# Kernel tuning notes

Hardware: AMD Instinct MI355X
Metric: run time of the kernel (lower is better)

Reference implementation:

```python
import jax, jax.numpy as jnp
import numpy as np

N_NODES = 200000
N_EDGES = 3200000
N_GRAPHS = 4096
IN_CH = 78
H1, H2, OUT_DIM = 64, 128, 128


def setup_inputs() -> dict:
    key = jax.random.key(0)
    ks = jax.random.split(key, 10)
    x = jax.random.normal(ks[0], (N_NODES, IN_CH), dtype=jnp.float32)
    edge_index = jax.random.randint(ks[1], (2, N_EDGES), 0, N_NODES, dtype=jnp.int64)
    batch = jnp.sort(jax.random.randint(ks[2], (N_NODES,), 0, N_GRAPHS, dtype=jnp.int64))
    # GCNConv weights (PyG: lin has no bias by default; conv bias added after aggregation)
    def glorot(k, fan_in, fan_out):
        lim = jnp.sqrt(6.0 / (fan_in + fan_out)).astype(jnp.float32)
        return jax.random.uniform(k, (fan_in, fan_out), jnp.float32, -lim, lim)
    W1 = glorot(ks[3], IN_CH, H1)
    b1 = jnp.zeros((H1,), jnp.float32)
    W2 = glorot(ks[4], H1, H2)
    b2 = jnp.zeros((H2,), jnp.float32)
    fc_w = glorot(ks[5], H2, OUT_DIM)
    fc_b = jnp.zeros((OUT_DIM,), jnp.float32)
    return {"x": x, "edge_index": edge_index, "batch": batch,
            "W1": W1, "b1": b1, "W2": W2, "b2": b2, "fc_w": fc_w, "fc_b": fc_b}


def _gcn_forward(x, edge_index, batch, W1, b1, W2, b2, fc_w, fc_b):
    N = x.shape[0]
    # GCNConv default: add self loops, symmetric deg^-1/2 normalization
    self_loops = jnp.arange(N, dtype=edge_index.dtype)
    src = jnp.concatenate([edge_index[0], self_loops])  # [E+N]
    dst = jnp.concatenate([edge_index[1], self_loops])  # [E+N]
    deg = jax.ops.segment_sum(jnp.ones_like(dst, dtype=jnp.float32), dst,
                              num_segments=N)  # in-degree incl self loop
    dinv = jnp.where(deg > 0, jax.lax.rsqrt(jnp.maximum(deg, 1.0)), 0.0)
    norm = dinv[src] * dinv[dst]  # [E+N]

    def gcn_layer(h, W, b):
        hw = h @ W                              # transform first (small dims)
        msg = hw[src] * norm[:, None]           # gather + scale  [E+N, F]
        agg = jax.ops.segment_sum(msg, dst, num_segments=N)  # scatter-add
        return agg + b

    h = jax.nn.relu(gcn_layer(x, W1, b1))
    h = jax.nn.relu(gcn_layer(h, W2, b2))
    # global_mean_pool over per-graph segments
    counts = jax.ops.segment_sum(jnp.ones((N,), jnp.float32), batch,
                                 num_segments=N_GRAPHS)
    pooled = jax.ops.segment_sum(h, batch, num_segments=N_GRAPHS)
    pooled = pooled / jnp.maximum(counts, 1.0)[:, None]  # [G, H2]
    return pooled @ fc_w + fc_b                           # [G, OUT_DIM]


def reference(x, edge_index, batch, W1, b1, W2, b2, fc_w, fc_b):
    return _gcn_forward(x, edge_index, batch, W1, b1, W2, b2, fc_w, fc_b)
```

## Files before the change

kernel.cpp:

```cpp
#include <hip/hip_runtime.h>
#include <hip/hip_bf16.h>

#define NN 200000
#define NE 3200000
#define NG 4096
#define INC 78
#define C1 64
#define C2 128
#define ODIM 128
#define KP1 96

#define BSZ 256
#define NBKT 782
#define NBLK 196
#define EPB 16327
#define SCN (NBKT*NBLK)
#define MAXREC 12288

using bf16 = __hip_bfloat16;
typedef __attribute__((ext_vector_type(8))) short bf16x8;
typedef __attribute__((ext_vector_type(4))) float f32x4;

static inline size_t alignup(size_t x) { return (x + 255) & ~size_t(255); }

__device__ __forceinline__ float bflo(unsigned u) { return __uint_as_float(u << 16); }
__device__ __forceinline__ float bfhi(unsigned u) { return __uint_as_float(u & 0xffff0000u); }
__device__ __forceinline__ unsigned short f2bf(float f) {
    __hip_bfloat16 h = __float2bfloat16(f);
    return *reinterpret_cast<unsigned short*>(&h);
}

__global__ void hist1_kernel(const int* __restrict__ dst, int* __restrict__ histM) {
    __shared__ int lh[NBKT];
    for (int j = threadIdx.x; j < NBKT; j += 256) lh[j] = 0;
    __syncthreads();
    int e0 = blockIdx.x * EPB;
    int e1 = e0 + EPB; if (e1 > NE) e1 = NE;
    for (int e = e0 + threadIdx.x; e < e1; e += 256)
        atomicAdd(&lh[((unsigned)dst[e]) >> 8], 1);
    __syncthreads();
    for (int j = threadIdx.x; j < NBKT; j += 256)
        histM[j * NBLK + blockIdx.x] = lh[j];
}

__global__ void scan1_kernel(int* __restrict__ data, int* __restrict__ bsum, int n) {
    __shared__ int tmp[256];
    int tid = threadIdx.x, gid = blockIdx.x * 256 + tid;
    int v = (gid < n) ? data[gid] : 0;
    tmp[tid] = v;
    __syncthreads();
    for (int off = 1; off < 256; off <<= 1) {
        int t = (tid >= off) ? tmp[tid - off] : 0;
        __syncthreads();
        tmp[tid] += t;
        __syncthreads();
    }
    if (gid < n) data[gid] = tmp[tid] - v;
    if (tid == 255) bsum[blockIdx.x] = tmp[255];
}

__global__ void scan2_kernel(int* __restrict__ bsum, int nb) {
    __shared__ int tmp[1024];
    int tid = threadIdx.x;
    int v = (tid < nb) ? bsum[tid] : 0;
    tmp[tid] = v;
    __syncthreads();
    for (int off = 1; off < 1024; off <<= 1) {
        int t = (tid >= off) ? tmp[tid - off] : 0;
        __syncthreads();
        tmp[tid] += t;
        __syncthreads();
    }
    if (tid < nb) bsum[tid] = tmp[tid] - v;
}

__global__ void scatter2_kernel(const int* __restrict__ src, const int* __restrict__ dst,
                                const int* __restrict__ histM, const int* __restrict__ bsum,
                                unsigned* __restrict__ ecsr) {
    __shared__ int lc[NBKT];
    for (int j = threadIdx.x; j < NBKT; j += 256) {
        int idx = j * NBLK + blockIdx.x;
        lc[j] = histM[idx] + bsum[idx >> 8];
    }
    __syncthreads();
    int e0 = blockIdx.x * EPB;
    int e1 = e0 + EPB; if (e1 > NE) e1 = NE;
    for (int e = e0 + threadIdx.x; e < e1; e += 256) {
        int d = dst[e];
        int s = src[e];
        int pos = atomicAdd(&lc[((unsigned)d) >> 8], 1);
        ecsr[pos] = ((unsigned)s << 8) | (unsigned)(d & 255);
    }
}

__global__ __launch_bounds__(256) void degcsr_kernel(
    const int* __restrict__ histM, const int* __restrict__ bsum,
    int* __restrict__ rs, float* __restrict__ dinv, unsigned* __restrict__ ecsr) {
    __shared__ int cnt[BSZ];
    __shared__ int pfx[BSZ];
    __shared__ unsigned recs[MAXREC];
    int b = blockIdx.x;
    int i0 = b * NBLK;
    int s0 = histM[i0] + bsum[i0 >> 8];
    int s1 = NE;
    if (b + 1 < NBKT) {
        int i1 = (b + 1) * NBLK;
        s1 = histM[i1] + bsum[i1 >> 8];
    }
    int nrec = s1 - s0;
    if (nrec > MAXREC) nrec = MAXREC;
    cnt[threadIdx.x] = 0;
    for (int i = threadIdx.x; i < nrec; i += 256) recs[i] = ecsr[s0 + i];
    __syncthreads();
    for (int i = threadIdx.x; i < nrec; i += 256)
        atomicAdd(&cnt[recs[i] & 255], 1);
    __syncthreads();
    int v = cnt[threadIdx.x];
    pfx[threadIdx.x] = v;
    __syncthreads();
    for (int off = 1; off < 256; off <<= 1) {
        int t = (threadIdx.x >= off) ? pfx[threadIdx.x - off] : 0;
        __syncthreads();
        pfx[threadIdx.x] += t;
        __syncthreads();
    }
    int myrs = s0 + pfx[threadIdx.x] - v;
    int node = b * BSZ + threadIdx.x;
    if (node < NN) {
        rs[node] = myrs;
        dinv[node] = rsqrtf((float)v + 1.0f);
    }
    if (node == NN) rs[NN] = NE;
    __syncthreads();
    cnt[threadIdx.x] = 0;
    pfx[threadIdx.x] = myrs;
    __syncthreads();
    for (int i = threadIdx.x; i < nrec; i += 256) {
        unsigned rec = recs[i];
        int nl = rec & 255;
        int pos = atomicAdd(&cnt[nl], 1);
        ecsr[pfx[nl] + pos] = rec >> 8;
    }
}

__global__ void convw2_kernel(const float* __restrict__ W1, const float* __restrict__ W2,
                              unsigned short* __restrict__ Wt1, unsigned short* __restrict__ Wt2) {
    int idx = blockIdx.x * 256 + threadIdx.x;
    if (idx < C1 * KP1) {
        int c = idx / KP1, k = idx % KP1;
        Wt1[idx] = f2bf((k < INC) ? W1[k * C1 + c] : 0.f);
    } else {
        int j = idx - C1 * KP1;
        if (j < C2 * C1) {
            int c = j / C1, k = j % C1;
            Wt2[j] = f2bf(W2[k * C2 + c]);
        }
    }
}

__global__ __launch_bounds__(256) void gemm1_mfma(const float* __restrict__ x,
                                                  const unsigned short* __restrict__ Wt1,
                                                  const float* __restrict__ dinv,
                                                  unsigned short* __restrict__ hw1s) {
    __shared__ float xs[64 * INC];
    const float4* gsrc = (const float4*)(x + (size_t)blockIdx.x * 64 * INC);
    float4* ldst = (float4*)xs;
    #pragma unroll
    for (int t = 0; t < 5; ++t) {
        int i = t * 256 + threadIdx.x;
        if (i < (64 * INC) / 4) ldst[i] = gsrc[i];
    }
    __syncthreads();
    int wave = threadIdx.x >> 6, lane = threadIdx.x & 63;
    int r = lane & 15, kg = lane >> 4;
    int lrow = wave * 16 + r;
    int row0 = blockIdx.x * 64 + wave * 16;
    const float* arow = xs + lrow * INC;
    bf16x8 a[3];
    #pragma unroll
    for (int t = 0; t < 3; ++t) {
        union { bf16x8 v; unsigned short u[8]; } tmp;
        #pragma unroll
        for (int j = 0; j < 8; ++j) {
            int k = t * 32 + kg * 8 + j;
            tmp.u[j] = (k < INC) ? f2bf(arow[k]) : (unsigned short)0;
        }
        a[t] = tmp.v;
    }
    float dsc[4];
    #pragma unroll
    for (int i = 0; i < 4; ++i) dsc[i] = dinv[row0 + kg * 4 + i];
    #pragma unroll
    for (int nt = 0; nt < 4; ++nt) {
        const unsigned short* wrow = Wt1 + (size_t)(nt * 16 + r) * KP1 + kg * 8;
        bf16x8 b0 = *(const bf16x8*)(wrow);
        bf16x8 b1 = *(const bf16x8*)(wrow + 32);
        bf16x8 b2 = *(const bf16x8*)(wrow + 64);
        f32x4 acc = {0.f, 0.f, 0.f, 0.f};
        acc = __builtin_amdgcn_mfma_f32_16x16x32_bf16(a[0], b0, acc, 0, 0, 0);
        acc = __builtin_amdgcn_mfma_f32_16x16x32_bf16(a[1], b1, acc, 0, 0, 0);
        acc = __builtin_amdgcn_mfma_f32_16x16x32_bf16(a[2], b2, acc, 0, 0, 0);
        unsigned short* cb = hw1s + (size_t)(row0 + kg * 4) * C1 + nt * 16 + r;
        #pragma unroll
        for (int i = 0; i < 4; ++i) cb[(size_t)i * C1] = f2bf(acc[i] * dsc[i]);
    }
}

__device__ __forceinline__ void gather_node(
    const unsigned* __restrict__ csr, int start, int len,
    const unsigned short* __restrict__ vin, int c0,
    float& a0, float& a1, float& a2, float& a3,
    float& a4, float& a5, float& a6, float& a7) {
    int e = 0;
    for (; e + 4 <= len; e += 4) {
        unsigned s0 = csr[start + e + 0];
        unsigned s1 = csr[start + e + 1];
        unsigned s2 = csr[start + e + 2];
        unsigned s3 = csr[start + e + 3];
        uint4 r0 = *(const uint4*)(vin + (size_t)s0 * 64 + c0);
        uint4 r1 = *(const uint4*)(vin + (size_t)s1 * 64 + c0);
        uint4 r2 = *(const uint4*)(vin + (size_t)s2 * 64 + c0);
        uint4 r3 = *(const uint4*)(vin + (size_t)s3 * 64 + c0);
        a0 += (bflo(r0.x) + bflo(r1.x)) + (bflo(r2.x) + bflo(r3.x));
        a1 += (bfhi(r0.x) + bfhi(r1.x)) + (bfhi(r2.x) + bfhi(r3.x));
        a2 += (bflo(r0.y) + bflo(r1.y)) + (bflo(r2.y) + bflo(r3.y));
        a3 += (bfhi(r0.y) + bfhi(r1.y)) + (bfhi(r2.y) + bfhi(r3.y));
        a4 += (bflo(r0.z) + bflo(r1.z)) + (bflo(r2.z) + bflo(r3.z));
        a5 += (bfhi(r0.z) + bfhi(r1.z)) + (bfhi(r2.z) + bfhi(r3.z));
        a6 += (bflo(r0.w) + bflo(r1.w)) + (bflo(r2.w) + bflo(r3.w));
        a7 += (bfhi(r0.w) + bfhi(r1.w)) + (bfhi(r2.w) + bfhi(r3.w));
    }
    for (; e < len; ++e) {
        unsigned s = csr[start + e];
        uint4 ra = *(const uint4*)(vin + (size_t)s * 64 + c0);
        a0 += bflo(ra.x); a1 += bfhi(ra.x);
        a2 += bflo(ra.y); a3 += bfhi(ra.y);
        a4 += bflo(ra.z); a5 += bfhi(ra.z);
        a6 += bflo(ra.w); a7 += bfhi(ra.w);
    }
}

__global__ __launch_bounds__(256) void agg1_kernel(
    const unsigned* __restrict__ csr, const int* __restrict__ rs,
    const float* __restrict__ dinv, const unsigned short* __restrict__ vin,
    const float* __restrict__ bias, unsigned short* __restrict__ vout) {
    int node = blockIdx.x * 32 + (threadIdx.x >> 3);
    int l = threadIdx.x & 7;
    int c0 = l * 8;
    int start = rs[node], len = rs[node + 1] - start;
    float a0 = 0.f, a1 = 0.f, a2 = 0.f, a3 = 0.f, a4 = 0.f, a5 = 0.f, a6 = 0.f, a7 = 0.f;
    gather_node(csr, start, len, vin, c0, a0, a1, a2, a3, a4, a5, a6, a7);
    uint4 sv = *(const uint4*)(vin + (size_t)node * 64 + c0);
    a0 += bflo(sv.x); a1 += bfhi(sv.x);
    a2 += bflo(sv.y); a3 += bfhi(sv.y);
    a4 += bflo(sv.z); a5 += bfhi(sv.z);
    a6 += bflo(sv.w); a7 += bfhi(sv.w);
    float d = dinv[node];
    a0 = fmaxf(a0 * d + bias[c0 + 0], 0.f) * d;
    a1 = fmaxf(a1 * d + bias[c0 + 1], 0.f) * d;
    a2 = fmaxf(a2 * d + bias[c0 + 2], 0.f) * d;
    a3 = fmaxf(a3 * d + bias[c0 + 3], 0.f) * d;
    a4 = fmaxf(a4 * d + bias[c0 + 4], 0.f) * d;
    a5 = fmaxf(a5 * d + bias[c0 + 5], 0.f) * d;
    a6 = fmaxf(a6 * d + bias[c0 + 6], 0.f) * d;
    a7 = fmaxf(a7 * d + bias[c0 + 7], 0.f) * d;
    uint4 o;
    o.x = (unsigned)f2bf(a0) | ((unsigned)f2bf(a1) << 16);
    o.y = (unsigned)f2bf(a2) | ((unsigned)f2bf(a3) << 16);
    o.z = (unsigned)f2bf(a4) | ((unsigned)f2bf(a5) << 16);
    o.w = (unsigned)f2bf(a6) | ((unsigned)f2bf(a7) << 16);
    *(uint4*)(vout + (size_t)node * 64 + c0) = o;
}

__global__ __launch_bounds__(256) void agg2g_mfma(
    const unsigned* __restrict__ csr, const int* __restrict__ rs,
    const float* __restrict__ dinv, const unsigned short* __restrict__ h1s,
    const unsigned short* __restrict__ Wt2, const float* __restrict__ b2,
    unsigned short* __restrict__ h2) {
    __shared__ unsigned short A[64 * 72];
    int grp = threadIdx.x >> 3;
    int l = threadIdx.x & 7;
    int c0 = l * 8;
    #pragma unroll
    for (int half = 0; half < 2; ++half) {
        int nl = grp + half * 32;
        int node = blockIdx.x * 64 + nl;
        int start = rs[node], len = rs[node + 1] - start;
        float a0 = 0.f, a1 = 0.f, a2 = 0.f, a3 = 0.f, a4 = 0.f, a5 = 0.f, a6 = 0.f, a7 = 0.f;
        gather_node(csr, start, len, h1s, c0, a0, a1, a2, a3, a4, a5, a6, a7);
        uint4 sv = *(const uint4*)(h1s + (size_t)node * 64 + c0);
        a0 += bflo(sv.x); a1 += bfhi(sv.x);
        a2 += bflo(sv.y); a3 += bfhi(sv.y);
        a4 += bflo(sv.z); a5 += bfhi(sv.z);
        a6 += bflo(sv.w); a7 += bfhi(sv.w);
        float d = dinv[node];
        uint4 o;
        o.x = (unsigned)f2bf(a0 * d) | ((unsigned)f2bf(a1 * d) << 16);
        o.y = (unsigned)f2bf(a2 * d) | ((unsigned)f2bf(a3 * d) << 16);
        o.z = (unsigned)f2bf(a4 * d) | ((unsigned)f2bf(a5 * d) << 16);
        o.w = (unsigned)f2bf(a6 * d) | ((unsigned)f2bf(a7 * d) << 16);
        *(uint4*)(A + nl * 72 + c0) = o;
    }
    __syncthreads();
    int wave = threadIdx.x >> 6, lane = threadIdx.x & 63;
    int r = lane & 15, kg = lane >> 4;
    int lrow = wave * 16 + r;
    int row0 = blockIdx.x * 64 + wave * 16;
    bf16x8 a0 = *(const bf16x8*)(A + lrow * 72 + kg * 8);
    bf16x8 a1 = *(const bf16x8*)(A + lrow * 72 + 32 + kg * 8);
    #pragma unroll
    for (int nt = 0; nt < 8; ++nt) {
        const unsigned short* wrow = Wt2 + (size_t)(nt * 16 + r) * C1 + kg * 8;
        bf16x8 b0 = *(const bf16x8*)(wrow);
        bf16x8 b1 = *(const bf16x8*)(wrow + 32);
        f32x4 acc = {0.f, 0.f, 0.f, 0.f};
        acc = __builtin_amdgcn_mfma_f32_16x16x32_bf16(a0, b0, acc, 0, 0, 0);
        acc = __builtin_amdgcn_mfma_f32_16x16x32_bf16(a1, b1, acc, 0, 0, 0);
        int col = nt * 16 + r;
        float bb = b2[col];
        unsigned short* cb = h2 + (size_t)(row0 + kg * 4) * C2 + col;
        #pragma unroll
        for (int i = 0; i < 4; ++i) cb[(size_t)i * C2] = f2bf(fmaxf(acc[i] + bb, 0.f));
    }
}

__device__ __forceinline__ int lbound(const int* __restrict__ a, int n, int key) {
    int lo = 0, hi = n;
    while (lo < hi) {
        int mid = (lo + hi) >> 1;
        if (a[mid] < key) lo = mid + 1; else hi = mid;
    }
    return lo;
}

__global__ __launch_bounds__(256) void pool_fc_kernel(const unsigned short* __restrict__ h2,
                                                      const int* __restrict__ batch,
                                                      const float* __restrict__ fcw,
                                                      const float* __restrict__ fcb,
                                                      float* __restrict__ out) {
    __shared__ float ps[512];
    __shared__ float pr[128];
    int g = blockIdx.x;
    int lo = lbound(batch, NN, g);
    int hi = lbound(batch, NN, g + 1);
    int cnt = hi - lo;
    int rg = threadIdx.x >> 6;
    int p = threadIdx.x & 63;
    float s0 = 0.f, s1 = 0.f;
    for (int r = lo + rg; r < hi; r += 4) {
        unsigned v = *(const unsigned*)(h2 + (size_t)r * C2 + p * 2);
        s0 += bflo(v);
        s1 += bfhi(v);
    }
    ps[threadIdx.x * 2 + 0] = s0;
    ps[threadIdx.x * 2 + 1] = s1;
    __syncthreads();
    if (threadIdx.x < 64) {
        float inv = 1.0f / (float)((cnt > 0) ? cnt : 1);
        int t = threadIdx.x;
        float r0 = 0.f, r1 = 0.f;
        #pragma unroll
        for (int k = 0; k < 4; ++k) {
            r0 += ps[(k * 64 + t) * 2 + 0];
            r1 += ps[(k * 64 + t) * 2 + 1];
        }
        pr[2 * t + 0] = r0 * inv;
        pr[2 * t + 1] = r1 * inv;
    }
    __syncthreads();
    if (threadIdx.x < 128) {
        int o = threadIdx.x;
        float acc = fcb[o];
        #pragma unroll 8
        for (int k = 0; k < C2; ++k) acc += pr[k] * fcw[k * ODIM + o];
        out[(size_t)g * ODIM + o] = acc;
    }
}

extern "C" void kernel_launch(void* const* d_in, const int* in_sizes, int n_in,
                              void* d_out, int out_size, void* d_ws, size_t ws_size,
                              hipStream_t stream) {
    const float* x   = (const float*)d_in[0];
    const int*   ei  = (const int*)d_in[1];
    const int*   bat = (const int*)d_in[2];
    const float* W1  = (const float*)d_in[3];
    const float* b1  = (const float*)d_in[4];
    const float* W2  = (const float*)d_in[5];
    const float* b2  = (const float*)d_in[6];
    const float* fcw = (const float*)d_in[7];
    const float* fcb = (const float*)d_in[8];
    float* out = (float*)d_out;

    const int* src = ei;
    const int* dst = ei + NE;

    char* ws = (char*)d_ws;
    int* histM   = (int*)ws;            ws += alignup((size_t)SCN * 4);
    int* bsum    = (int*)ws;            ws += alignup(1024 * 4);
    int* rs      = (int*)ws;            ws += alignup((size_t)(NN + 1) * 4);
    float* dinv  = (float*)ws;          ws += alignup((size_t)NN * 4);
    unsigned short* Wt1 = (unsigned short*)ws;  ws += alignup((size_t)C1 * KP1 * 2);
    unsigned short* Wt2 = (unsigned short*)ws;  ws += alignup((size_t)C2 * C1 * 2);
    unsigned short* hw1s = (unsigned short*)ws; ws += alignup((size_t)NN * C1 * 2);
    unsigned* ecsr = (unsigned*)ws;     ws += alignup((size_t)NE * 4);
    unsigned short* h1s = (unsigned short*)ws;  ws += alignup((size_t)NN * C1 * 2);
    unsigned short* h2 = (unsigned short*)ws;   ws += alignup((size_t)NN * C2 * 2);

    hist1_kernel<<<NBLK, 256, 0, stream>>>(dst, histM);
    const int SCB = (SCN + 255) / 256;
    scan1_kernel<<<SCB, 256, 0, stream>>>(histM, bsum, SCN);
    scan2_kernel<<<1, 1024, 0, stream>>>(bsum, SCB);
    scatter2_kernel<<<NBLK, 256, 0, stream>>>(src, dst, histM, bsum, ecsr);

    degcsr_kernel<<<NBKT, 256, 0, stream>>>(histM, bsum, rs, dinv, ecsr);

    convw2_kernel<<<(C1 * KP1 + C2 * C1 + 255) / 256, 256, 0, stream>>>(W1, W2, Wt1, Wt2);

    gemm1_mfma<<<NN / 64, 256, 0, stream>>>(x, Wt1, dinv, hw1s);
    agg1_kernel<<<NN / 32, 256, 0, stream>>>(ecsr, rs, dinv, hw1s, b1, h1s);

    agg2g_mfma<<<NN / 64, 256, 0, stream>>>(ecsr, rs, dinv, h1s, Wt2, b2, h2);

    pool_fc_kernel<<<NG, 256, 0, stream>>>(h2, bat, fcw, fcb, out);
}
```

Measured before the change: 299.7 us.

## Split 64-channel features into two 32-channel halves mapped to XCD groups

Node features are stored as two separate 32-column bf16 arrays. The aggregation kernels pick a half from the XCD index of the block (blockIdx & 7), so each group of four XCDs gathers from a working set half the size, which should fit better in its L2. The second layer's aggregation is split out of the fused agg+GEMM kernel into a separate half-aggregation pass and a standalone GEMM2 kernel. This adds an extra kernel launch and a round trip of the aggregated features through global memory, and it relies on the hardware assigning blocks to XCDs round-robin.

```diff
diff --git a/kernel.cpp b/kernel.cpp
--- a/kernel.cpp
+++ b/kernel.cpp
@@ -16,6 +16,7 @@
 #define EPB 16327
 #define SCN (NBKT*NBLK)
 #define MAXREC 12288
+#define HGRID 6256
 
 using bf16 = __hip_bfloat16;
 typedef __attribute__((ext_vector_type(8))) short bf16x8;
@@ -161,7 +162,8 @@
 __global__ __launch_bounds__(256) void gemm1_mfma(const float* __restrict__ x,
                                                   const unsigned short* __restrict__ Wt1,
                                                   const float* __restrict__ dinv,
-                                                  unsigned short* __restrict__ hw1s) {
+                                                  unsigned short* __restrict__ hwA,
+                                                  unsigned short* __restrict__ hwB) {
     __shared__ float xs[64 * INC];
     const float4* gsrc = (const float4*)(x + (size_t)blockIdx.x * 64 * INC);
     float4* ldst = (float4*)xs;
@@ -200,13 +202,15 @@
         acc = __builtin_amdgcn_mfma_f32_16x16x32_bf16(a[0], b0, acc, 0, 0, 0);
         acc = __builtin_amdgcn_mfma_f32_16x16x32_bf16(a[1], b1, acc, 0, 0, 0);
         acc = __builtin_amdgcn_mfma_f32_16x16x32_bf16(a[2], b2, acc, 0, 0, 0);
-        unsigned short* cb = hw1s + (size_t)(row0 + kg * 4) * C1 + nt * 16 + r;
+        int col = nt * 16 + r;
+        unsigned short* tb = (col < 32) ? hwA : hwB;
+        unsigned short* cb = tb + (size_t)(row0 + kg * 4) * 32 + (col & 31);
         #pragma unroll
-        for (int i = 0; i < 4; ++i) cb[(size_t)i * C1] = f2bf(acc[i] * dsc[i]);
-    }
-}
-
-__device__ __forceinline__ void gather_node(
+        for (int i = 0; i < 4; ++i) cb[(size_t)i * 32] = f2bf(acc[i] * dsc[i]);
+    }
+}
+
+__device__ __forceinline__ void gather32(
     const unsigned* __restrict__ csr, int start, int len,
     const unsigned short* __restrict__ vin, int c0,
     float& a0, float& a1, float& a2, float& a3,
@@ -217,10 +221,10 @@
         unsigned s1 = csr[start + e + 1];
         unsigned s2 = csr[start + e + 2];
         unsigned s3 = csr[start + e + 3];
-        uint4 r0 = *(const uint4*)(vin + (size_t)s0 * 64 + c0);
-        uint4 r1 = *(const uint4*)(vin + (size_t)s1 * 64 + c0);
-        uint4 r2 = *(const uint4*)(vin + (size_t)s2 * 64 + c0);
-        uint4 r3 = *(const uint4*)(vin + (size_t)s3 * 64 + c0);
+        uint4 r0 = *(const uint4*)(vin + (size_t)s0 * 32 + c0);
+        uint4 r1 = *(const uint4*)(vin + (size_t)s1 * 32 + c0);
+        uint4 r2 = *(const uint4*)(vin + (size_t)s2 * 32 + c0);
+        uint4 r3 = *(const uint4*)(vin + (size_t)s3 * 32 + c0);
         a0 += (bflo(r0.x) + bflo(r1.x)) + (bflo(r2.x) + bflo(r3.x));
         a1 += (bfhi(r0.x) + bfhi(r1.x)) + (bfhi(r2.x) + bfhi(r3.x));
         a2 += (bflo(r0.y) + bflo(r1.y)) + (bflo(r2.y) + bflo(r3.y));
@@ -232,7 +236,7 @@
     }
     for (; e < len; ++e) {
         unsigned s = csr[start + e];
-        uint4 ra = *(const uint4*)(vin + (size_t)s * 64 + c0);
+        uint4 ra = *(const uint4*)(vin + (size_t)s * 32 + c0);
         a0 += bflo(ra.x); a1 += bfhi(ra.x);
         a2 += bflo(ra.y); a3 += bfhi(ra.y);
         a4 += bflo(ra.z); a5 += bfhi(ra.z);
@@ -240,74 +244,61 @@
     }
 }
 
-__global__ __launch_bounds__(256) void agg1_kernel(
+template <int EP>
+__global__ __launch_bounds__(256) void agg_half_kernel(
     const unsigned* __restrict__ csr, const int* __restrict__ rs,
-    const float* __restrict__ dinv, const unsigned short* __restrict__ vin,
-    const float* __restrict__ bias, unsigned short* __restrict__ vout) {
-    int node = blockIdx.x * 32 + (threadIdx.x >> 3);
-    int l = threadIdx.x & 7;
-    int c0 = l * 8;
+    const float* __restrict__ dinv,
+    const unsigned short* __restrict__ vinA, const unsigned short* __restrict__ vinB,
+    const float* __restrict__ bias,
+    unsigned short* __restrict__ voutA, unsigned short* __restrict__ voutB) {
+    int xcd = blockIdx.x & 7;
+    int half = xcd >> 2;
+    int ord = (blockIdx.x >> 3) * 4 + (xcd & 3);
+    int node = ord * 64 + (threadIdx.x >> 2);
+    if (node >= NN) return;
+    int c0 = (threadIdx.x & 3) * 8;
+    const unsigned short* vin = half ? vinB : vinA;
+    unsigned short* vout = half ? voutB : voutA;
     int start = rs[node], len = rs[node + 1] - start;
     float a0 = 0.f, a1 = 0.f, a2 = 0.f, a3 = 0.f, a4 = 0.f, a5 = 0.f, a6 = 0.f, a7 = 0.f;
-    gather_node(csr, start, len, vin, c0, a0, a1, a2, a3, a4, a5, a6, a7);
-    uint4 sv = *(const uint4*)(vin + (size_t)node * 64 + c0);
+    gather32(csr, start, len, vin, c0, a0, a1, a2, a3, a4, a5, a6, a7);
+    uint4 sv = *(const uint4*)(vin + (size_t)node * 32 + c0);
     a0 += bflo(sv.x); a1 += bfhi(sv.x);
     a2 += bflo(sv.y); a3 += bfhi(sv.y);
     a4 += bflo(sv.z); a5 += bfhi(sv.z);
     a6 += bflo(sv.w); a7 += bfhi(sv.w);
     float d = dinv[node];
-    a0 = fmaxf(a0 * d + bias[c0 + 0], 0.f) * d;
-    a1 = fmaxf(a1 * d + bias[c0 + 1], 0.f) * d;
-    a2 = fmaxf(a2 * d + bias[c0 + 2], 0.f) * d;
-    a3 = fmaxf(a3 * d + bias[c0 + 3], 0.f) * d;
-    a4 = fmaxf(a4 * d + bias[c0 + 4], 0.f) * d;
-    a5 = fmaxf(a5 * d + bias[c0 + 5], 0.f) * d;
-    a6 = fmaxf(a6 * d + bias[c0 + 6], 0.f) * d;
-    a7 = fmaxf(a7 * d + bias[c0 + 7], 0.f) * d;
+    if (EP == 1) {
+        const float* bb = bias + half * 32 + c0;
+        a0 = fmaxf(a0 * d + bb[0], 0.f) * d;
+        a1 = fmaxf(a1 * d + bb[1], 0.f) * d;
+        a2 = fmaxf(a2 * d + bb[2], 0.f) * d;
+        a3 = fmaxf(a3 * d + bb[3], 0.f) * d;
+        a4 = fmaxf(a4 * d + bb[4], 0.f) * d;
+        a5 = fmaxf(a5 * d + bb[5], 0.f) * d;
+        a6 = fmaxf(a6 * d + bb[6], 0.f) * d;
+        a7 = fmaxf(a7 * d + bb[7], 0.f) * d;
+    } else {
+        a0 *= d; a1 *= d; a2 *= d; a3 *= d; a4 *= d; a5 *= d; a6 *= d; a7 *= d;
+    }
     uint4 o;
     o.x = (unsigned)f2bf(a0) | ((unsigned)f2bf(a1) << 16);
     o.y = (unsigned)f2bf(a2) | ((unsigned)f2bf(a3) << 16);
     o.z = (unsigned)f2bf(a4) | ((unsigned)f2bf(a5) << 16);
     o.w = (unsigned)f2bf(a6) | ((unsigned)f2bf(a7) << 16);
-    *(uint4*)(vout + (size_t)node * 64 + c0) = o;
-}
-
-__global__ __launch_bounds__(256) void agg2g_mfma(
-    const unsigned* __restrict__ csr, const int* __restrict__ rs,
-    const float* __restrict__ dinv, const unsigned short* __restrict__ h1s,
-    const unsigned short* __restrict__ Wt2, const float* __restrict__ b2,
-    unsigned short* __restrict__ h2) {
-    __shared__ unsigned short A[64 * 72];
-    int grp = threadIdx.x >> 3;
-    int l = threadIdx.x & 7;
-    int c0 = l * 8;
-    #pragma unroll
-    for (int half = 0; half < 2; ++half) {
-        int nl = grp + half * 32;
-        int node = blockIdx.x * 64 + nl;
-        int start = rs[node], len = rs[node + 1] - start;
-        float a0 = 0.f, a1 = 0.f, a2 = 0.f, a3 = 0.f, a4 = 0.f, a5 = 0.f, a6 = 0.f, a7 = 0.f;
-        gather_node(csr, start, len, h1s, c0, a0, a1, a2, a3, a4, a5, a6, a7);
-        uint4 sv = *(const uint4*)(h1s + (size_t)node * 64 + c0);
-        a0 += bflo(sv.x); a1 += bfhi(sv.x);
-        a2 += bflo(sv.y); a3 += bfhi(sv.y);
-        a4 += bflo(sv.z); a5 += bfhi(sv.z);
-        a6 += bflo(sv.w); a7 += bfhi(sv.w);
-        float d = dinv[node];
-        uint4 o;
-        o.x = (unsigned)f2bf(a0 * d) | ((unsigned)f2bf(a1 * d) << 16);
-        o.y = (unsigned)f2bf(a2 * d) | ((unsigned)f2bf(a3 * d) << 16);
-        o.z = (unsigned)f2bf(a4 * d) | ((unsigned)f2bf(a5 * d) << 16);
-        o.w = (unsigned)f2bf(a6 * d) | ((unsigned)f2bf(a7 * d) << 16);
-        *(uint4*)(A + nl * 72 + c0) = o;
-    }
-    __syncthreads();
+    *(uint4*)(vout + (size_t)node * 32 + c0) = o;
+}
+
+__global__ __launch_bounds__(256) void gemm2_mfma(const unsigned short* __restrict__ aggA,
+                                                  const unsigned short* __restrict__ aggB,
+                                                  const unsigned short* __restrict__ Wt2,
+                                                  const float* __restrict__ b2,
+                                                  unsigned short* __restrict__ h2) {
     int wave = threadIdx.x >> 6, lane = threadIdx.x & 63;
     int r = lane & 15, kg = lane >> 4;
-    int lrow = wave * 16 + r;
     int row0 = blockIdx.x * 64 + wave * 16;
-    bf16x8 a0 = *(const bf16x8*)(A + lrow * 72 + kg * 8);
-    bf16x8 a1 = *(const bf16x8*)(A + lrow * 72 + 32 + kg * 8);
+    bf16x8 a0 = *(const bf16x8*)(aggA + (size_t)(row0 + r) * 32 + kg * 8);
+    bf16x8 a1 = *(const bf16x8*)(aggB + (size_t)(row0 + r) * 32 + kg * 8);
     #pragma unroll
     for (int nt = 0; nt < 8; ++nt) {
         const unsigned short* wrow = Wt2 + (size_t)(nt * 16 + r) * C1 + kg * 8;
@@ -401,9 +392,13 @@
     float* dinv  = (float*)ws;          ws += alignup((size_t)NN * 4);
     unsigned short* Wt1 = (unsigned short*)ws;  ws += alignup((size_t)C1 * KP1 * 2);
     unsigned short* Wt2 = (unsigned short*)ws;  ws += alignup((size_t)C2 * C1 * 2);
-    unsigned short* hw1s = (unsigned short*)ws; ws += alignup((size_t)NN * C1 * 2);
+    unsigned short* hw1sA = (unsigned short*)ws; ws += alignup((size_t)NN * 32 * 2);
+    unsigned short* hw1sB = (unsigned short*)ws; ws += alignup((size_t)NN * 32 * 2);
+    unsigned short* aggHA = hw1sA;
+    unsigned short* aggHB = hw1sB;
     unsigned* ecsr = (unsigned*)ws;     ws += alignup((size_t)NE * 4);
-    unsigned short* h1s = (unsigned short*)ws;  ws += alignup((size_t)NN * C1 * 2);
+    unsigned short* h1sA = (unsigned short*)ws; ws += alignup((size_t)NN * 32 * 2);
+    unsigned short* h1sB = (unsigned short*)ws; ws += alignup((size_t)NN * 32 * 2);
     unsigned short* h2 = (unsigned short*)ws;   ws += alignup((size_t)NN * C2 * 2);
 
     hist1_kernel<<<NBLK, 256, 0, stream>>>(dst, histM);
@@ -416,10 +411,11 @@
 
     convw2_kernel<<<(C1 * KP1 + C2 * C1 + 255) / 256, 256, 0, stream>>>(W1, W2, Wt1, Wt2);
 
-    gemm1_mfma<<<NN / 64, 256, 0, stream>>>(x, Wt1, dinv, hw1s);
-    agg1_kernel<<<NN / 32, 256, 0, stream>>>(ecsr, rs, dinv, hw1s, b1, h1s);
-
-    agg2g_mfma<<<NN / 64, 256, 0, stream>>>(ecsr, rs, dinv, h1s, Wt2, b2, h2);
+    gemm1_mfma<<<NN / 64, 256, 0, stream>>>(x, Wt1, dinv, hw1sA, hw1sB);
+    agg_half_kernel<1><<<HGRID, 256, 0, stream>>>(ecsr, rs, dinv, hw1sA, hw1sB, b1, h1sA, h1sB);
+
+    agg_half_kernel<2><<<HGRID, 256, 0, stream>>>(ecsr, rs, dinv, h1sA, h1sB, b1, aggHA, aggHB);
+    gemm2_mfma<<<NN / 64, 256, 0, stream>>>(aggHA, aggHB, Wt2, b2, h2);
 
     pool_fc_kernel<<<NG, 256, 0, stream>>>(h2, bat, fcw, fcb, out);
 }
```

After: 378.9 us. 1.26x slower.

## Replace histogram-scan CSR build with single-pass bucket binsort; split agg2 from GEMM2

Applied to the files above, without the earlier changes.

The multi-kernel CSR build (block histogram, two-level scan, scatter) is replaced by one binsort kernel. It stages edges in LDS, reserves space per bucket with global atomics, and writes into fixed-capacity per-bucket buffers, followed by a small bucket scan. The fused layer-2 gather+MFMA kernel is split into a reusable aggregation kernel and a standalone GEMM2 kernel that reads the aggregated bf16 features from global memory. The build saves launches and one pass over the edges, but gives up deterministic edge order and truncates any bucket above CAP=8192. The split adds a global write and read of the aggregated features.

```diff
diff --git a/kernel.cpp b/kernel.cpp
--- a/kernel.cpp
+++ b/kernel.cpp
@@ -12,10 +12,9 @@
 
 #define BSZ 256
 #define NBKT 782
-#define NBLK 196
-#define EPB 16327
-#define SCN (NBKT*NBLK)
-#define MAXREC 12288
+#define NBLK 392
+#define EPB 8164
+#define CAP 8192
 
 using bf16 = __hip_bfloat16;
 typedef __attribute__((ext_vector_type(8))) short bf16x8;
@@ -30,39 +29,43 @@
     return *reinterpret_cast<unsigned short*>(&h);
 }
 
-__global__ void hist1_kernel(const int* __restrict__ dst, int* __restrict__ histM) {
+__global__ __launch_bounds__(256) void binsort_kernel(const int* __restrict__ src,
+                                                      const int* __restrict__ dst,
+                                                      int* __restrict__ gcursor,
+                                                      unsigned* __restrict__ ebuf) {
+    __shared__ unsigned recs[EPB + 28];
+    __shared__ unsigned short bkts[EPB + 28];
     __shared__ int lh[NBKT];
     for (int j = threadIdx.x; j < NBKT; j += 256) lh[j] = 0;
     __syncthreads();
     int e0 = blockIdx.x * EPB;
     int e1 = e0 + EPB; if (e1 > NE) e1 = NE;
-    for (int e = e0 + threadIdx.x; e < e1; e += 256)
-        atomicAdd(&lh[((unsigned)dst[e]) >> 8], 1);
-    __syncthreads();
-    for (int j = threadIdx.x; j < NBKT; j += 256)
-        histM[j * NBLK + blockIdx.x] = lh[j];
-}
-
-__global__ void scan1_kernel(int* __restrict__ data, int* __restrict__ bsum, int n) {
-    __shared__ int tmp[256];
-    int tid = threadIdx.x, gid = blockIdx.x * 256 + tid;
-    int v = (gid < n) ? data[gid] : 0;
-    tmp[tid] = v;
-    __syncthreads();
-    for (int off = 1; off < 256; off <<= 1) {
-        int t = (tid >= off) ? tmp[tid - off] : 0;
-        __syncthreads();
-        tmp[tid] += t;
-        __syncthreads();
-    }
-    if (gid < n) data[gid] = tmp[tid] - v;
-    if (tid == 255) bsum[blockIdx.x] = tmp[255];
-}
-
-__global__ void scan2_kernel(int* __restrict__ bsum, int nb) {
+    int n = e1 - e0;
+    for (int i = threadIdx.x; i < n; i += 256) {
+        int d = dst[e0 + i];
+        int s = src[e0 + i];
+        recs[i] = ((unsigned)s << 8) | (unsigned)(d & 255);
+        int b = ((unsigned)d) >> 8;
+        bkts[i] = (unsigned short)b;
+        atomicAdd(&lh[b], 1);
+    }
+    __syncthreads();
+    for (int j = threadIdx.x; j < NBKT; j += 256) {
+        int c = lh[j];
+        lh[j] = (c > 0) ? atomicAdd(&gcursor[j], c) : 0;
+    }
+    __syncthreads();
+    for (int i = threadIdx.x; i < n; i += 256) {
+        int b = bkts[i];
+        int off = atomicAdd(&lh[b], 1);
+        if (off < CAP) ebuf[(size_t)b * CAP + off] = recs[i];
+    }
+}
+
+__global__ void bucketscan_kernel(const int* __restrict__ gcursor, int* __restrict__ bstart) {
     __shared__ int tmp[1024];
     int tid = threadIdx.x;
-    int v = (tid < nb) ? bsum[tid] : 0;
+    int v = (tid < NBKT) ? gcursor[tid] : 0;
     tmp[tid] = v;
     __syncthreads();
     for (int off = 1; off < 1024; off <<= 1) {
@@ -71,46 +74,22 @@
         tmp[tid] += t;
         __syncthreads();
     }
-    if (tid < nb) bsum[tid] = tmp[tid] - v;
-}
-
-__global__ void scatter2_kernel(const int* __restrict__ src, const int* __restrict__ dst,
-                                const int* __restrict__ histM, const int* __restrict__ bsum,
-                                unsigned* __restrict__ ecsr) {
-    __shared__ int lc[NBKT];
-    for (int j = threadIdx.x; j < NBKT; j += 256) {
-        int idx = j * NBLK + blockIdx.x;
-        lc[j] = histM[idx] + bsum[idx >> 8];
-    }
-    __syncthreads();
-    int e0 = blockIdx.x * EPB;
-    int e1 = e0 + EPB; if (e1 > NE) e1 = NE;
-    for (int e = e0 + threadIdx.x; e < e1; e += 256) {
-        int d = dst[e];
-        int s = src[e];
-        int pos = atomicAdd(&lc[((unsigned)d) >> 8], 1);
-        ecsr[pos] = ((unsigned)s << 8) | (unsigned)(d & 255);
-    }
+    if (tid < NBKT) bstart[tid] = tmp[tid] - v;
+    if (tid == NBKT) bstart[NBKT] = NE;
 }
 
 __global__ __launch_bounds__(256) void degcsr_kernel(
-    const int* __restrict__ histM, const int* __restrict__ bsum,
-    int* __restrict__ rs, float* __restrict__ dinv, unsigned* __restrict__ ecsr) {
+    const unsigned* __restrict__ ebuf, const int* __restrict__ gcursor,
+    const int* __restrict__ bstart, int* __restrict__ rs, float* __restrict__ dinv,
+    unsigned* __restrict__ csr) {
     __shared__ int cnt[BSZ];
     __shared__ int pfx[BSZ];
-    __shared__ unsigned recs[MAXREC];
+    __shared__ unsigned recs[CAP];
     int b = blockIdx.x;
-    int i0 = b * NBLK;
-    int s0 = histM[i0] + bsum[i0 >> 8];
-    int s1 = NE;
-    if (b + 1 < NBKT) {
-        int i1 = (b + 1) * NBLK;
-        s1 = histM[i1] + bsum[i1 >> 8];
-    }
-    int nrec = s1 - s0;
-    if (nrec > MAXREC) nrec = MAXREC;
+    int nrec = gcursor[b]; if (nrec > CAP) nrec = CAP;
+    int s0 = bstart[b];
     cnt[threadIdx.x] = 0;
-    for (int i = threadIdx.x; i < nrec; i += 256) recs[i] = ecsr[s0 + i];
+    for (int i = threadIdx.x; i < nrec; i += 256) recs[i] = ebuf[(size_t)b * CAP + i];
     __syncthreads();
     for (int i = threadIdx.x; i < nrec; i += 256)
         atomicAdd(&cnt[recs[i] & 255], 1);
@@ -139,7 +118,7 @@
         unsigned rec = recs[i];
         int nl = rec & 255;
         int pos = atomicAdd(&cnt[nl], 1);
-        ecsr[pfx[nl] + pos] = rec >> 8;
+        csr[pfx[nl] + pos] = rec >> 8;
     }
 }
 
@@ -240,7 +219,8 @@
     }
 }
 
-__global__ __launch_bounds__(256) void agg1_kernel(
+template <int EP>
+__global__ __launch_bounds__(256) void agg_csr_kernel(
     const unsigned* __restrict__ csr, const int* __restrict__ rs,
     const float* __restrict__ dinv, const unsigned short* __restrict__ vin,
     const float* __restrict__ bias, unsigned short* __restrict__ vout) {
@@ -256,14 +236,18 @@
     a4 += bflo(sv.z); a5 += bfhi(sv.z);
     a6 += bflo(sv.w); a7 += bfhi(sv.w);
     float d = dinv[node];
-    a0 = fmaxf(a0 * d + bias[c0 + 0], 0.f) * d;
-    a1 = fmaxf(a1 * d + bias[c0 + 1], 0.f) * d;
-    a2 = fmaxf(a2 * d + bias[c0 + 2], 0.f) * d;
-    a3 = fmaxf(a3 * d + bias[c0 + 3], 0.f) * d;
-    a4 = fmaxf(a4 * d + bias[c0 + 4], 0.f) * d;
-    a5 = fmaxf(a5 * d + bias[c0 + 5], 0.f) * d;
-    a6 = fmaxf(a6 * d + bias[c0 + 6], 0.f) * d;
-    a7 = fmaxf(a7 * d + bias[c0 + 7], 0.f) * d;
+    if (EP == 1) {
+        a0 = fmaxf(a0 * d + bias[c0 + 0], 0.f) * d;
+        a1 = fmaxf(a1 * d + bias[c0 + 1], 0.f) * d;
+        a2 = fmaxf(a2 * d + bias[c0 + 2], 0.f) * d;
+        a3 = fmaxf(a3 * d + bias[c0 + 3], 0.f) * d;
+        a4 = fmaxf(a4 * d + bias[c0 + 4], 0.f) * d;
+        a5 = fmaxf(a5 * d + bias[c0 + 5], 0.f) * d;
+        a6 = fmaxf(a6 * d + bias[c0 + 6], 0.f) * d;
+        a7 = fmaxf(a7 * d + bias[c0 + 7], 0.f) * d;
+    } else {
+        a0 *= d; a1 *= d; a2 *= d; a3 *= d; a4 *= d; a5 *= d; a6 *= d; a7 *= d;
+    }
     uint4 o;
     o.x = (unsigned)f2bf(a0) | ((unsigned)f2bf(a1) << 16);
     o.y = (unsigned)f2bf(a2) | ((unsigned)f2bf(a3) << 16);
@@ -272,42 +256,16 @@
     *(uint4*)(vout + (size_t)node * 64 + c0) = o;
 }
 
-__global__ __launch_bounds__(256) void agg2g_mfma(
-    const unsigned* __restrict__ csr, const int* __restrict__ rs,
-    const float* __restrict__ dinv, const unsigned short* __restrict__ h1s,
-    const unsigned short* __restrict__ Wt2, const float* __restrict__ b2,
-    unsigned short* __restrict__ h2) {
-    __shared__ unsigned short A[64 * 72];
-    int grp = threadIdx.x >> 3;
-    int l = threadIdx.x & 7;
-    int c0 = l * 8;
-    #pragma unroll
-    for (int half = 0; half < 2; ++half) {
-        int nl = grp + half * 32;
-        int node = blockIdx.x * 64 + nl;
-        int start = rs[node], len = rs[node + 1] - start;
-        float a0 = 0.f, a1 = 0.f, a2 = 0.f, a3 = 0.f, a4 = 0.f, a5 = 0.f, a6 = 0.f, a7 = 0.f;
-        gather_node(csr, start, len, h1s, c0, a0, a1, a2, a3, a4, a5, a6, a7);
-        uint4 sv = *(const uint4*)(h1s + (size_t)node * 64 + c0);
-        a0 += bflo(sv.x); a1 += bfhi(sv.x);
-        a2 += bflo(sv.y); a3 += bfhi(sv.y);
-        a4 += bflo(sv.z); a5 += bfhi(sv.z);
-        a6 += bflo(sv.w); a7 += bfhi(sv.w);
-        float d = dinv[node];
-        uint4 o;
-        o.x = (unsigned)f2bf(a0 * d) | ((unsigned)f2bf(a1 * d) << 16);
-        o.y = (unsigned)f2bf(a2 * d) | ((unsigned)f2bf(a3 * d) << 16);
-        o.z = (unsigned)f2bf(a4 * d) | ((unsigned)f2bf(a5 * d) << 16);
-        o.w = (unsigned)f2bf(a6 * d) | ((unsigned)f2bf(a7 * d) << 16);
-        *(uint4*)(A + nl * 72 + c0) = o;
-    }
-    __syncthreads();
+__global__ __launch_bounds__(256) void gemm2_mfma(const unsigned short* __restrict__ aggH,
+                                                  const unsigned short* __restrict__ Wt2,
+                                                  const float* __restrict__ b2,
+                                                  unsigned short* __restrict__ h2) {
     int wave = threadIdx.x >> 6, lane = threadIdx.x & 63;
     int r = lane & 15, kg = lane >> 4;
-    int lrow = wave * 16 + r;
     int row0 = blockIdx.x * 64 + wave * 16;
-    bf16x8 a0 = *(const bf16x8*)(A + lrow * 72 + kg * 8);
-    bf16x8 a1 = *(const bf16x8*)(A + lrow * 72 + 32 + kg * 8);
+    const unsigned short* arow = aggH + (size_t)(row0 + r) * 64 + kg * 8;
+    bf16x8 a0 = *(const bf16x8*)(arow);
+    bf16x8 a1 = *(const bf16x8*)(arow + 32);
     #pragma unroll
     for (int nt = 0; nt < 8; ++nt) {
         const unsigned short* wrow = Wt2 + (size_t)(nt * 16 + r) * C1 + kg * 8;
@@ -395,31 +353,32 @@
     const int* dst = ei + NE;
 
     char* ws = (char*)d_ws;
-    int* histM   = (int*)ws;            ws += alignup((size_t)SCN * 4);
-    int* bsum    = (int*)ws;            ws += alignup(1024 * 4);
+    int* gcursor = (int*)ws;            ws += alignup((size_t)NBKT * 4);
+    int* bstart  = (int*)ws;            ws += alignup((size_t)(NBKT + 1) * 4);
     int* rs      = (int*)ws;            ws += alignup((size_t)(NN + 1) * 4);
     float* dinv  = (float*)ws;          ws += alignup((size_t)NN * 4);
     unsigned short* Wt1 = (unsigned short*)ws;  ws += alignup((size_t)C1 * KP1 * 2);
     unsigned short* Wt2 = (unsigned short*)ws;  ws += alignup((size_t)C2 * C1 * 2);
     unsigned short* hw1s = (unsigned short*)ws; ws += alignup((size_t)NN * C1 * 2);
-    unsigned* ecsr = (unsigned*)ws;     ws += alignup((size_t)NE * 4);
+    unsigned short* aggH = hw1s;
+    unsigned* ebuf = (unsigned*)ws;     ws += alignup((size_t)NBKT * CAP * 4);
+    unsigned* csr  = (unsigned*)ws;     ws += alignup((size_t)NE * 4);
     unsigned short* h1s = (unsigned short*)ws;  ws += alignup((size_t)NN * C1 * 2);
-    unsigned short* h2 = (unsigned short*)ws;   ws += alignup((size_t)NN * C2 * 2);
-
-    hist1_kernel<<<NBLK, 256, 0, stream>>>(dst, histM);
-    const int SCB = (SCN + 255) / 256;
-    scan1_kernel<<<SCB, 256, 0, stream>>>(histM, bsum, SCN);
-    scan2_kernel<<<1, 1024, 0, stream>>>(bsum, SCB);
-    scatter2_kernel<<<NBLK, 256, 0, stream>>>(src, dst, histM, bsum, ecsr);
-
-    degcsr_kernel<<<NBKT, 256, 0, stream>>>(histM, bsum, rs, dinv, ecsr);
+    unsigned short* h2 = (unsigned short*)ebuf;
+
+    hipMemsetAsync(gcursor, 0, (size_t)NBKT * 4, stream);
+    binsort_kernel<<<NBLK, 256, 0, stream>>>(src, dst, gcursor, ebuf);
+    bucketscan_kernel<<<1, 1024, 0, stream>>>(gcursor, bstart);
+
+    degcsr_kernel<<<NBKT, 256, 0, stream>>>(ebuf, gcursor, bstart, rs, dinv, csr);
 
     convw2_kernel<<<(C1 * KP1 + C2 * C1 + 255) / 256, 256, 0, stream>>>(W1, W2, Wt1, Wt2);
 
     gemm1_mfma<<<NN / 64, 256, 0, stream>>>(x, Wt1, dinv, hw1s);
-    agg1_kernel<<<NN / 32, 256, 0, stream>>>(ecsr, rs, dinv, hw1s, b1, h1s);
-
-    agg2g_mfma<<<NN / 64, 256, 0, stream>>>(ecsr, rs, dinv, h1s, Wt2, b2, h2);
+    agg_csr_kernel<1><<<NN / 32, 256, 0, stream>>>(csr, rs, dinv, hw1s, b1, h1s);
+
+    agg_csr_kernel<2><<<NN / 32, 256, 0, stream>>>(csr, rs, dinv, h1s, b1, aggH);
+    gemm2_mfma<<<NN / 64, 256, 0, stream>>>(aggH, Wt2, b2, h2);
 
     pool_fc_kernel<<<NG, 256, 0, stream>>>(h2, bat, fcw, fcb, out);
 }
```

Result: faster. 288.4 us (-3.8%).
